# Optimization experiments

Hardware: AMD Instinct MI355X
Metric: run time of the kernel (lower is better)

The kernel has to match this reference:

```python
import jax, jax.numpy as jnp
import numpy as np
import math

B, L, D = 4, 1024, 1024
A, H = 1024, 16
DH = A // H  # head_size = 64
SCALE = 1.0 / math.sqrt(D)  # note: module scales by sqrt(input_size), not head_size
LN_EPS = 1e-5


def setup_inputs() -> dict:
    key = jax.random.key(0)
    ks = jax.random.split(key, 10)
    def xavier(k, fan_in, fan_out):
        lim = math.sqrt(6.0 / (fan_in + fan_out))
        return jax.random.uniform(k, (fan_out, fan_in), jnp.float32, -lim, lim)
    return {
        "x": jax.random.normal(ks[0], (B, L, D), jnp.float32),
        "queries": jax.random.normal(ks[1], (B, L, D), jnp.float32),
        "Wk": xavier(ks[2], D, A),
        "Wq_self": xavier(ks[3], D, A),
        "Wq_other": xavier(ks[4], D, A),
        "Wv": xavier(ks[5], D, A),
        "Wo": xavier(ks[6], A, A),
        "bo": jnp.zeros((A,), jnp.float32),
        "gamma": jnp.ones((A,), jnp.float32),
        "beta": jnp.zeros((A,), jnp.float32),
        "attention_mask": jnp.ones((B, L), jnp.int32),
    }


def reference(x, queries, Wk, Wq_self, Wq_other, Wv, Wo, bo, gamma, beta, attention_mask):
    # projections (Linear: y = x @ W.T), split heads to (B, L, H, DH)
    def proj(inp, W):
        return (inp @ W.T).reshape(B, L, H, DH)
    k = proj(x, Wk)
    q_self = proj(x, Wq_self)
    q_other = proj(queries, Wq_other)
    v = proj(x, Wv)

    # scores_self + scores_other == (q_self + q_other) @ k^T  (algebraically identical)
    q_comb = q_self + q_other
    scores = jnp.einsum("bqhd,bkhd->bhqk", q_comb, k) * SCALE  # (B, H, L, L)

    # mask: (B, L) -> (B, 1, 1, L) broadcast over heads and query positions
    m = attention_mask.astype(scores.dtype)[:, None, None, :]
    scores = scores + (1.0 - m) * -100000.0

    attn = jax.nn.softmax(scores, axis=-1)  # dropout p=0 -> identity

    out = jnp.einsum("bhqk,bkhd->bqhd", attn, v).reshape(B, L, A)

    # FF output: Linear -> identity activation -> LayerNorm (dropout=0)
    out = out @ Wo.T + bo
    mu = jnp.mean(out, axis=-1, keepdims=True)
    var = jnp.var(out, axis=-1, keepdims=True)
    out = (out - mu) * jax.lax.rsqrt(var + LN_EPS) * gamma + beta
    return out
```

## Files before the change

kernel.cpp:

```cpp
#include <hip/hip_runtime.h>
#include <hip/hip_bf16.h>
#include <math.h>

#define BB 4
#define LL 1024
#define DD 1024
#define AA 1024
#define HH 16
#define DHH 64
#define LOG2E 1.44269504f
#define QSC 0.045084223f
#define MBIAS -144269.5f

typedef __attribute__((ext_vector_type(8))) short short8;
typedef __attribute__((ext_vector_type(4))) float floatx4;

__device__ __forceinline__ float bf2f(unsigned short u) {
    union { unsigned u; float f; } x; x.u = ((unsigned)u) << 16; return x.f;
}
__device__ __forceinline__ unsigned short f2bf(float f) {
    union { float f; unsigned u; } x; x.f = f;
    unsigned r = x.u + 0x7fffu + ((x.u >> 16) & 1u);
    return (unsigned short)(r >> 16);
}
__device__ __forceinline__ unsigned pkbf(float a, float b) {
    union { __hip_bfloat162 h; unsigned u; } c;
    c.h = __float22bfloat162_rn(make_float2(a, b));
    return c.u;
}

__device__ __forceinline__ void gload16(const void* g, const void* l) {
    __builtin_amdgcn_global_load_lds(
        (const __attribute__((address_space(1))) unsigned int*)g,
        (__attribute__((address_space(3))) unsigned int*)l, 16, 0, 0);
}

__device__ __forceinline__ void remap8(int& bx, int& by) {
    const int lin = blockIdx.x + (blockIdx.y << 4);
    const int xcd = lin & 7, f = lin >> 3;
    by = ((xcd >> 1) << 3) + (f >> 3);
    bx = ((xcd & 1) << 3) + (f & 7);
}

struct ConvDesc { const float* s[8]; unsigned short* d[8]; };

__global__ __launch_bounds__(256) void conv_f2b(ConvDesc cd) {
    const int u  = blockIdx.x >> 10;
    const int lb = blockIdx.x & 1023;
    const int idx = lb * 1024 + threadIdx.x * 4;
    float4 v = *reinterpret_cast<const float4*>(cd.s[u] + idx);
    uint2 o;
    o.x = pkbf(v.x, v.y);
    o.y = pkbf(v.z, v.w);
    *reinterpret_cast<uint2*>(cd.d[u] + idx) = o;
}

__device__ __forceinline__ void gemm_pass(const unsigned short* A, const float* B,
                                          int mblk, int nblk,
                                          int kbase, int ksteps,
                                          unsigned short* As, unsigned short* Bs,
                                          floatx4 (&acc)[4][2])
{
    const int tid  = threadIdx.x;
    const int lane = tid & 63;
    const int l16  = lane & 15;
    const int quad = lane >> 4;
    const int wave = tid >> 6;
    const int wm = wave >> 1, wn = wave & 1;
    const int arow = wave * 8 + (lane >> 3);
    const int acol = ((lane & 7) ^ (lane >> 3)) << 3;
    const int brow = tid >> 3;
    const int bcol = (tid & 7) << 3;
    const int bslot = ((tid & 7) ^ (brow & 7)) << 3;

    float4 br[4];
    {
        const float* p0 = B + (size_t)(nblk + brow) * DD + kbase + bcol;
        const float* p1 = B + (size_t)(nblk + brow + 32) * DD + kbase + bcol;
        br[0] = ((const float4*)p0)[0]; br[1] = ((const float4*)p0)[1];
        br[2] = ((const float4*)p1)[0]; br[3] = ((const float4*)p1)[1];
    }

    for (int s = 0; s < ksteps; ++s) {
        const int k0 = kbase + s * 64;
        __syncthreads();
        for (int is = 0; is < 4; ++is)
            gload16(A + (size_t)(mblk + is * 32 + arow) * DD + k0 + acol,
                    As + is * 2048 + wave * 512);
        {
            uint4 t0, t1;
            t0.x = pkbf(br[0].x, br[0].y); t0.y = pkbf(br[0].z, br[0].w);
            t0.z = pkbf(br[1].x, br[1].y); t0.w = pkbf(br[1].z, br[1].w);
            t1.x = pkbf(br[2].x, br[2].y); t1.y = pkbf(br[2].z, br[2].w);
            t1.z = pkbf(br[3].x, br[3].y); t1.w = pkbf(br[3].z, br[3].w);
            *reinterpret_cast<uint4*>(Bs + brow * 64 + bslot) = t0;
            *reinterpret_cast<uint4*>(Bs + (brow + 32) * 64 + bslot) = t1;
        }
        __syncthreads();
        if (s + 1 < ksteps) {
            const int nk = k0 + 64;
            const float* p0 = B + (size_t)(nblk + brow) * DD + nk + bcol;
            const float* p1 = B + (size_t)(nblk + brow + 32) * DD + nk + bcol;
            br[0] = ((const float4*)p0)[0]; br[1] = ((const float4*)p0)[1];
            br[2] = ((const float4*)p1)[0]; br[3] = ((const float4*)p1)[1];
        }
        for (int kh = 0; kh < 2; ++kh) {
            const int sl = ((kh * 4 + quad) ^ (l16 & 7)) << 3;
            short8 af[4], bfr[2];
            for (int i = 0; i < 4; ++i)
                af[i] = *reinterpret_cast<const short8*>(
                    As + (wm * 64 + i * 16 + l16) * 64 + sl);
            for (int j = 0; j < 2; ++j)
                bfr[j] = *reinterpret_cast<const short8*>(
                    Bs + (wn * 32 + j * 16 + l16) * 64 + sl);
            for (int i = 0; i < 4; ++i)
                for (int j = 0; j < 2; ++j)
                    acc[i][j] = __builtin_amdgcn_mfma_f32_16x16x32_bf16(
                        af[i], bfr[j], acc[i][j], 0, 0, 0);
        }
    }
}

__device__ __forceinline__ void store_nat(floatx4 (&acc)[4][2], unsigned short* As,
                                          unsigned short* C, int mblk, int nblk)
{
    const int lane = threadIdx.x & 63;
    const int l16  = lane & 15;
    const int quad = lane >> 4;
    const int wave = threadIdx.x >> 6;
    const int wm = wave >> 1, wn = wave & 1;
    __syncthreads();
    unsigned short* Cw = As + wave * 2048;
    for (int i = 0; i < 4; ++i)
        for (int j = 0; j < 2; ++j)
            for (int r = 0; r < 4; ++r)
                Cw[(i * 16 + quad * 4 + r) * 32 + j * 16 + l16] = f2bf(acc[i][j][r]);
    __asm__ volatile("s_waitcnt lgkmcnt(0)" ::: "memory");
    const int mb = mblk + wm * 64;
    const int nb = nblk + wn * 32;
    for (int s = 0; s < 4; ++s) {
        const int row = s * 16 + (lane >> 2);
        uint4 v = *reinterpret_cast<const uint4*>(Cw + row * 32 + (lane & 3) * 8);
        *reinterpret_cast<uint4*>(C + (size_t)(mb + row) * AA + nb + (lane & 3) * 8) = v;
    }
}

__device__ __forceinline__ void store_vt(floatx4 (&acc)[4][2], unsigned short* As,
                                         unsigned short* vt, int mblk, int h)
{
    const int lane = threadIdx.x & 63;
    const int l16  = lane & 15;
    const int quad = lane >> 4;
    const int wave = threadIdx.x >> 6;
    const int wm = wave >> 1, wn = wave & 1;
    __syncthreads();
    unsigned short* Cw = As + wave * 2048;
    for (int i = 0; i < 4; ++i)
        for (int j = 0; j < 2; ++j) {
            ushort4 pv;
            pv.x = f2bf(acc[i][j][0]); pv.y = f2bf(acc[i][j][1]);
            pv.z = f2bf(acc[i][j][2]); pv.w = f2bf(acc[i][j][3]);
            *reinterpret_cast<ushort4*>(&Cw[(j * 16 + l16) * 64 + i * 16 + quad * 4]) = pv;
        }
    __asm__ volatile("s_waitcnt lgkmcnt(0)" ::: "memory");
    const int mg = mblk + wm * 64;
    const int b  = mg >> 10, lbase = mg & 1023;
    for (int s = 0; s < 4; ++s) {
        const int drow = s * 8 + (lane >> 3);
        uint4 v = *reinterpret_cast<const uint4*>(Cw + drow * 64 + (lane & 7) * 8);
        *reinterpret_cast<uint4*>(
            vt + (size_t)((b * HH + h) * DHH + wn * 32 + drow) * LL + lbase + (lane & 7) * 8) = v;
    }
}

__global__ __launch_bounds__(256) void gemm_proj3(
    const unsigned short* __restrict__ xb, const unsigned short* __restrict__ qb,
    const float* __restrict__ Wqs, const float* __restrict__ Wqo,
    const float* __restrict__ Wk, const float* __restrict__ Wv,
    unsigned short* __restrict__ qc, unsigned short* __restrict__ kk,
    unsigned short* __restrict__ vt)
{
    __shared__ alignas(16) unsigned short As[128 * 64];
    __shared__ alignas(16) unsigned short Bs[64 * 64];
    floatx4 acc[4][2] = {};
    int bx, by; remap8(bx, by);
    const int mblk = by * 128, nblk = bx * 64;
    if (blockIdx.z == 0) {
        gemm_pass(xb, Wqs, mblk, nblk, 0, 16, As, Bs, acc);
        gemm_pass(qb, Wqo, mblk, nblk, 0, 16, As, Bs, acc);
        store_nat(acc, As, qc, mblk, nblk);
    } else if (blockIdx.z == 1) {
        gemm_pass(xb, Wk, mblk, nblk, 0, 16, As, Bs, acc);
        store_nat(acc, As, kk, mblk, nblk);
    } else {
        gemm_pass(xb, Wv, mblk, nblk, 0, 16, As, Bs, acc);
        store_vt(acc, As, vt, mblk, bx);
    }
}

__global__ __launch_bounds__(256) void gemm_projqk(
    const unsigned short* __restrict__ xb, const unsigned short* __restrict__ qb,
    const float* __restrict__ Wqs, const float* __restrict__ Wqo,
    const float* __restrict__ Wk,
    unsigned short* __restrict__ qc, unsigned short* __restrict__ kk)
{
    __shared__ alignas(16) unsigned short As[128 * 64];
    __shared__ alignas(16) unsigned short Bs[64 * 64];
    floatx4 acc[4][2] = {};
    int bx, by; remap8(bx, by);
    const int mblk = by * 128, nblk = bx * 64;
    if (blockIdx.z == 0) {
        gemm_pass(xb, Wqs, mblk, nblk, 0, 16, As, Bs, acc);
        gemm_pass(qb, Wqo, mblk, nblk, 0, 16, As, Bs, acc);
        store_nat(acc, As, qc, mblk, nblk);
    } else {
        gemm_pass(xb, Wk, mblk, nblk, 0, 16, As, Bs, acc);
        store_nat(acc, As, kk, mblk, nblk);
    }
}

__global__ __launch_bounds__(256) void gemm_v(
    const unsigned short* __restrict__ xb, const float* __restrict__ Wv,
    unsigned short* __restrict__ vt)
{
    __shared__ alignas(16) unsigned short As[128 * 64];
    __shared__ alignas(16) unsigned short Bs[64 * 64];
    floatx4 acc[4][2] = {};
    int bx, by; remap8(bx, by);
    gemm_pass(xb, Wv, by * 128, bx * 64, 0, 16, As, Bs, acc);
    store_vt(acc, As, vt, by * 128, bx);
}

__global__ __launch_bounds__(256) void gemm_wo(
    const unsigned short* __restrict__ ao, const float* __restrict__ Wo,
    unsigned short* __restrict__ pj0, unsigned short* __restrict__ pj1)
{
    __shared__ alignas(16) unsigned short As[128 * 64];
    __shared__ alignas(16) unsigned short Bs[64 * 64];
    floatx4 acc[4][2] = {};
    int bx, by; remap8(bx, by);
    const int z = blockIdx.z;
    gemm_pass(ao, Wo, by * 128, bx * 64, z * 512, 8, As, Bs, acc);
    store_nat(acc, As, z ? pj1 : pj0, by * 128, bx * 64);
}

__device__ __forceinline__ int swzb(int row, int slot) {
    return (row << 7) + ((slot ^ (row & 7)) << 4);
}

__global__ __launch_bounds__(256, 4) void attn_flash(const unsigned short* qc,
                                                     const unsigned short* __restrict__ kmat,
                                                     const unsigned short* __restrict__ vt,
                                                     const int* __restrict__ mask,
                                                     unsigned short* ao)
{
    const int blk = blockIdx.x;
    const int xcd = blk & 7;
    const int sub = blk >> 3;
    const int bh  = xcd * 8 + (sub >> 4);
    const int qt  = sub & 15;
    const int b   = bh >> 4;
    const int h   = bh & 15;

    const int wave = threadIdx.x >> 6;
    const int lane = threadIdx.x & 63;
    const int l16  = lane & 15;
    const int quad = lane >> 4;
    const int q0 = qt * 64 + wave * 16;

    __shared__ alignas(16) unsigned short Ks[2][64 * 64];
    __shared__ alignas(16) unsigned short Vs[2][64 * 64];
    __shared__ float Ml[LL];

    const int* bm = mask + b * LL;
    for (int i = 0; i < 4; ++i) {
        const int c = threadIdx.x + i * 256;
        Ml[c] = (1.0f - (float)bm[c]) * MBIAS;
    }

    short8 aq[2];
    for (int s = 0; s < 2; ++s) {
        const unsigned short* p =
            qc + (size_t)(b * LL + q0 + l16) * AA + h * DHH + s * 32 + quad * 8;
        short8 t = *reinterpret_cast<const short8*>(p);
        for (int e = 0; e < 8; ++e)
            t[e] = (short)f2bf(bf2f((unsigned short)t[e]) * QSC);
        aq[s] = t;
    }

    floatx4 O[4] = {};
    float lp = 0.f;

    const unsigned short* kbase = kmat + (size_t)(b * LL) * AA + h * DHH;
    const unsigned short* vbase = vt + (size_t)((b * HH + h) * DHH) * LL;
    const int c0 = threadIdx.x, c1 = threadIdx.x + 256;
    const int row0 = c0 >> 3, slot0 = c0 & 7;
    const int row1 = c1 >> 3, slot1 = c1 & 7;

    uint4 kr0, kr1, vr0, vr1;
    kr0 = *reinterpret_cast<const uint4*>(kbase + (size_t)row0 * AA + slot0 * 8);
    kr1 = *reinterpret_cast<const uint4*>(kbase + (size_t)row1 * AA + slot1 * 8);
    vr0 = *reinterpret_cast<const uint4*>(vbase + (size_t)row0 * LL + slot0 * 8);
    vr1 = *reinterpret_cast<const uint4*>(vbase + (size_t)row1 * LL + slot1 * 8);
    *reinterpret_cast<uint4*>((char*)Ks[0] + swzb(row0, slot0)) = kr0;
    *reinterpret_cast<uint4*>((char*)Ks[0] + swzb(row1, slot1)) = kr1;
    *reinterpret_cast<uint4*>((char*)Vs[0] + swzb(row0, slot0)) = vr0;
    *reinterpret_cast<uint4*>((char*)Vs[0] + swzb(row1, slot1)) = vr1;
    {
        const unsigned short* kb1 = kbase + (size_t)64 * AA;
        const unsigned short* vb1 = vbase + 64;
        kr0 = *reinterpret_cast<const uint4*>(kb1 + (size_t)row0 * AA + slot0 * 8);
        kr1 = *reinterpret_cast<const uint4*>(kb1 + (size_t)row1 * AA + slot1 * 8);
        vr0 = *reinterpret_cast<const uint4*>(vb1 + (size_t)row0 * LL + slot0 * 8);
        vr1 = *reinterpret_cast<const uint4*>(vb1 + (size_t)row1 * LL + slot1 * 8);
    }
    __syncthreads();

    const int srcA = ((quad & 1) << 5) + l16;
    const int srcB = srcA + 16;
    const bool hi = quad >= 2;
    int cur = 0;

    for (int t = 0; t < 16; ++t) {
        const char* Kc = (const char*)Ks[cur];
        const char* Vc = (const char*)Vs[cur];
        if (t + 1 < 16) {
            char* Kn = (char*)Ks[cur ^ 1];
            char* Vn = (char*)Vs[cur ^ 1];
            *reinterpret_cast<uint4*>(Kn + swzb(row0, slot0)) = kr0;
            *reinterpret_cast<uint4*>(Kn + swzb(row1, slot1)) = kr1;
            *reinterpret_cast<uint4*>(Vn + swzb(row0, slot0)) = vr0;
            *reinterpret_cast<uint4*>(Vn + swzb(row1, slot1)) = vr1;
        }
        if (t + 2 < 16) {
            const unsigned short* kb2 = kbase + (size_t)(t + 2) * 64 * AA;
            const unsigned short* vb2 = vbase + (t + 2) * 64;
            kr0 = *reinterpret_cast<const uint4*>(kb2 + (size_t)row0 * AA + slot0 * 8);
            kr1 = *reinterpret_cast<const uint4*>(kb2 + (size_t)row1 * AA + slot1 * 8);
            vr0 = *reinterpret_cast<const uint4*>(vb2 + (size_t)row0 * LL + slot0 * 8);
            vr1 = *reinterpret_cast<const uint4*>(vb2 + (size_t)row1 * LL + slot1 * 8);
        }

        floatx4 p[4];
        const float* Mlb = Ml + t * 64 + quad * 4;
        for (int j = 0; j < 4; ++j) {
            const int rr = j * 16 + l16;
            const short8 kf0 = *reinterpret_cast<const short8*>(Kc + swzb(rr, quad));
            const short8 kf1 = *reinterpret_cast<const short8*>(Kc + swzb(rr, quad + 4));
            floatx4 s_ = {0.f, 0.f, 0.f, 0.f};
            s_ = __builtin_amdgcn_mfma_f32_16x16x32_bf16(kf0, aq[0], s_, 0, 0, 0);
            s_ = __builtin_amdgcn_mfma_f32_16x16x32_bf16(kf1, aq[1], s_, 0, 0, 0);
            const float4 mv = *reinterpret_cast<const float4*>(Mlb + j * 16);
            p[j][0] = exp2f(s_[0] + mv.x);
            p[j][1] = exp2f(s_[1] + mv.y);
            p[j][2] = exp2f(s_[2] + mv.z);
            p[j][3] = exp2f(s_[3] + mv.w);
            lp += (p[j][0] + p[j][1]) + (p[j][2] + p[j][3]);
        }
        unsigned pk[4][2];
        for (int j = 0; j < 4; ++j) {
            pk[j][0] = pkbf(p[j][0], p[j][1]);
            pk[j][1] = pkbf(p[j][2], p[j][3]);
        }
        union { unsigned u[4]; short8 s; } ap0, ap1;
        {
            unsigned xA0 = __shfl((int)pk[0][0], srcA), yA0 = __shfl((int)pk[1][0], srcA);
            unsigned xA1 = __shfl((int)pk[0][1], srcA), yA1 = __shfl((int)pk[1][1], srcA);
            unsigned xB0 = __shfl((int)pk[0][0], srcB), yB0 = __shfl((int)pk[1][0], srcB);
            unsigned xB1 = __shfl((int)pk[0][1], srcB), yB1 = __shfl((int)pk[1][1], srcB);
            ap0.u[0] = hi ? yA0 : xA0;
            ap0.u[1] = hi ? yA1 : xA1;
            ap0.u[2] = hi ? yB0 : xB0;
            ap0.u[3] = hi ? yB1 : xB1;
        }
        {
            unsigned xA0 = __shfl((int)pk[2][0], srcA), yA0 = __shfl((int)pk[3][0], srcA);
            unsigned xA1 = __shfl((int)pk[2][1], srcA), yA1 = __shfl((int)pk[3][1], srcA);
            unsigned xB0 = __shfl((int)pk[2][0], srcB), yB0 = __shfl((int)pk[3][0], srcB);
            unsigned xB1 = __shfl((int)pk[2][1], srcB), yB1 = __shfl((int)pk[3][1], srcB);
            ap1.u[0] = hi ? yA0 : xA0;
            ap1.u[1] = hi ? yA1 : xA1;
            ap1.u[2] = hi ? yB0 : xB0;
            ap1.u[3] = hi ? yB1 : xB1;
        }
        for (int t4 = 0; t4 < 4; ++t4) {
            const int rr = t4 * 16 + l16;
            const short8 bv0 = *reinterpret_cast<const short8*>(Vc + swzb(rr, quad));
            const short8 bv1 = *reinterpret_cast<const short8*>(Vc + swzb(rr, quad + 4));
            O[t4] = __builtin_amdgcn_mfma_f32_16x16x32_bf16(ap0.s, bv0, O[t4], 0, 0, 0);
            O[t4] = __builtin_amdgcn_mfma_f32_16x16x32_bf16(ap1.s, bv1, O[t4], 0, 0, 0);
        }
        __syncthreads();
        cur ^= 1;
    }

    lp += __shfl_xor(lp, 16);
    lp += __shfl_xor(lp, 32);
    float linv[4];
    for (int r = 0; r < 4; ++r) {
        const float s = __shfl(lp, quad * 4 + r);
        linv[r] = 1.0f / s;
    }
    for (int t4 = 0; t4 < 4; ++t4)
        for (int r = 0; r < 4; ++r)
            ao[(size_t)(b * LL + q0 + quad * 4 + r) * AA + h * DHH + t4 * 16 + l16] =
                f2bf(O[t4][r] * linv[r]);
}

__global__ __launch_bounds__(256) void ln_f32(const unsigned short* __restrict__ X0,
                                              const unsigned short* __restrict__ X1,
                                              const float* __restrict__ bo,
                                              const float* __restrict__ gamma,
                                              const float* __restrict__ beta,
                                              float* __restrict__ out)
{
    const int row = blockIdx.x;
    const unsigned short* x0 = X0 + (size_t)row * AA;
    const unsigned short* x1 = X1 + (size_t)row * AA;
    float v[4];
    float s = 0.f, s2 = 0.f;
    for (int e = 0; e < 4; ++e) {
        const int c = threadIdx.x + e * 256;
        const float f = bf2f(x0[c]) + bf2f(x1[c]) + bo[c];
        v[e] = f; s += f; s2 += f * f;
    }
    for (int d = 1; d < 64; d <<= 1) { s += __shfl_xor(s, d); s2 += __shfl_xor(s2, d); }
    __shared__ float red[4][2];
    const int wave = threadIdx.x >> 6;
    const int lane = threadIdx.x & 63;
    if (lane == 0) { red[wave][0] = s; red[wave][1] = s2; }
    __syncthreads();
    s  = red[0][0] + red[1][0] + red[2][0] + red[3][0];
    s2 = red[0][1] + red[1][1] + red[2][1] + red[3][1];
    const float mean = s * (1.0f / AA);
    const float var  = s2 * (1.0f / AA) - mean * mean;
    const float rstd = rsqrtf(var + 1e-5f);
    for (int e = 0; e < 4; ++e) {
        const int c = threadIdx.x + e * 256;
        out[(size_t)row * AA + c] = (v[e] - mean) * rstd * gamma[c] + beta[c];
    }
}

extern "C" void kernel_launch(void* const* d_in, const int* in_sizes, int n_in,
                              void* d_out, int out_size, void* d_ws, size_t ws_size,
                              hipStream_t stream)
{
    const float* x     = (const float*)d_in[0];
    const float* qrs   = (const float*)d_in[1];
    const float* Wk    = (const float*)d_in[2];
    const float* Wqs   = (const float*)d_in[3];
    const float* Wqo   = (const float*)d_in[4];
    const float* Wv    = (const float*)d_in[5];
    const float* Wo    = (const float*)d_in[6];
    const float* bo    = (const float*)d_in[7];
    const float* gamma = (const float*)d_in[8];
    const float* beta  = (const float*)d_in[9];
    const int*   mask  = (const int*)d_in[10];

    char* ws = (char*)d_ws;
    unsigned short* xb = (unsigned short*)(ws + (size_t)0);
    unsigned short* qb = (unsigned short*)(ws + ((size_t)8 << 20));
    const bool big = ws_size >= ((size_t)24 << 20);
    unsigned short* vt = big ? (unsigned short*)(ws + ((size_t)16 << 20)) : qb;
    unsigned short* qc = (unsigned short*)d_out;
    unsigned short* kk = (unsigned short*)((char*)d_out + ((size_t)8 << 20));
    unsigned short* ao  = qc;
    unsigned short* pj0 = xb;
    unsigned short* pj1 = kk;

    ConvDesc cd;
    for (int i = 0; i < 4; ++i) {
        cd.s[i]     = x   + (size_t)i * (1u << 20); cd.d[i]     = xb + (size_t)i * (1u << 20);
        cd.s[i + 4] = qrs + (size_t)i * (1u << 20); cd.d[i + 4] = qb + (size_t)i * (1u << 20);
    }
    conv_f2b<<<8 * 1024, 256, 0, stream>>>(cd);

    if (big) {
        dim3 g3(AA / 64, (BB * LL) / 128, 3);
        gemm_proj3<<<g3, 256, 0, stream>>>(xb, qb, Wqs, Wqo, Wk, Wv, qc, kk, vt);
    } else {
        dim3 g2(AA / 64, (BB * LL) / 128, 2);
        dim3 g1(AA / 64, (BB * LL) / 128);
        gemm_projqk<<<g2, 256, 0, stream>>>(xb, qb, Wqs, Wqo, Wk, qc, kk);
        gemm_v<<<g1, 256, 0, stream>>>(xb, Wv, vt);
    }
    attn_flash<<<BB * HH * (LL / 64), 256, 0, stream>>>(qc, kk, vt, mask, ao);
    dim3 gw(AA / 64, (BB * LL) / 128, 2);
    gemm_wo<<<gw, 256, 0, stream>>>(ao, Wo, pj0, pj1);
    ln_f32<<<BB * LL, 256, 0, stream>>>(pj0, pj1, bo, gamma, beta, (float*)d_out);
}
```

Before: 235.4 us.

## Widen projection GEMM tiles to 128x128 with per-wave 64x64 outputs

```diff
diff --git a/kernel.cpp b/kernel.cpp
--- a/kernel.cpp
+++ b/kernel.cpp
@@ -42,6 +42,13 @@
     bx = ((xcd & 1) << 3) + (f & 7);
 }
 
+__device__ __forceinline__ void remap128(int& bx, int& by) {
+    const int lin = blockIdx.x + (blockIdx.y << 3);
+    const int xcd = lin & 7, f = lin >> 3;
+    bx = ((xcd & 1) << 2) + (f & 3);
+    by = ((xcd >> 1) << 3) + (f >> 2);
+}
+
 struct ConvDesc { const float* s[8]; unsigned short* d[8]; };
 
 __global__ __launch_bounds__(256) void conv_f2b(ConvDesc cd) {
@@ -53,6 +60,195 @@
     o.x = pkbf(v.x, v.y);
     o.y = pkbf(v.z, v.w);
     *reinterpret_cast<uint2*>(cd.d[u] + idx) = o;
+}
+
+__device__ __forceinline__ void gemm_pass128(const unsigned short* A, const float* B,
+                                             int mblk, int nblk,
+                                             int kbase, int ksteps,
+                                             unsigned short* As, unsigned short* Bs,
+                                             floatx4 (&acc)[4][4])
+{
+    const int tid  = threadIdx.x;
+    const int lane = tid & 63;
+    const int l16  = lane & 15;
+    const int quad = lane >> 4;
+    const int wave = tid >> 6;
+    const int wm = wave >> 1, wn = wave & 1;
+    const int arow = wave * 8 + (lane >> 3);
+    const int acol = ((lane & 7) ^ (lane >> 3)) << 3;
+    const int brow = tid >> 3;
+    const int bcol = (tid & 7) << 3;
+    const int bslot = ((tid & 7) ^ (brow & 7)) << 3;
+
+    const unsigned short* ap = A + (size_t)(mblk + arow) * DD + kbase + acol;
+    const float* bp0 = B + (size_t)(nblk + brow) * DD + kbase + bcol;
+    const float* bp1 = bp0 + (size_t)32 * DD;
+    const float* bp2 = bp0 + (size_t)64 * DD;
+    const float* bp3 = bp0 + (size_t)96 * DD;
+
+    float4 br[8];
+    br[0] = ((const float4*)bp0)[0]; br[1] = ((const float4*)bp0)[1];
+    br[2] = ((const float4*)bp1)[0]; br[3] = ((const float4*)bp1)[1];
+    br[4] = ((const float4*)bp2)[0]; br[5] = ((const float4*)bp2)[1];
+    br[6] = ((const float4*)bp3)[0]; br[7] = ((const float4*)bp3)[1];
+
+    for (int s = 0; s < ksteps; ++s) {
+        __syncthreads();
+        for (int is = 0; is < 4; ++is)
+            gload16(ap + (size_t)(is * 32) * DD, As + is * 2048 + wave * 512);
+        {
+            uint4 t;
+            t.x = pkbf(br[0].x, br[0].y); t.y = pkbf(br[0].z, br[0].w);
+            t.z = pkbf(br[1].x, br[1].y); t.w = pkbf(br[1].z, br[1].w);
+            *reinterpret_cast<uint4*>(Bs + brow * 64 + bslot) = t;
+            t.x = pkbf(br[2].x, br[2].y); t.y = pkbf(br[2].z, br[2].w);
+            t.z = pkbf(br[3].x, br[3].y); t.w = pkbf(br[3].z, br[3].w);
+            *reinterpret_cast<uint4*>(Bs + (brow + 32) * 64 + bslot) = t;
+            t.x = pkbf(br[4].x, br[4].y); t.y = pkbf(br[4].z, br[4].w);
+            t.z = pkbf(br[5].x, br[5].y); t.w = pkbf(br[5].z, br[5].w);
+            *reinterpret_cast<uint4*>(Bs + (brow + 64) * 64 + bslot) = t;
+            t.x = pkbf(br[6].x, br[6].y); t.y = pkbf(br[6].z, br[6].w);
+            t.z = pkbf(br[7].x, br[7].y); t.w = pkbf(br[7].z, br[7].w);
+            *reinterpret_cast<uint4*>(Bs + (brow + 96) * 64 + bslot) = t;
+        }
+        __syncthreads();
+        if (s + 1 < ksteps) {
+            bp0 += 64; bp1 += 64; bp2 += 64; bp3 += 64;
+            br[0] = ((const float4*)bp0)[0]; br[1] = ((const float4*)bp0)[1];
+            br[2] = ((const float4*)bp1)[0]; br[3] = ((const float4*)bp1)[1];
+            br[4] = ((const float4*)bp2)[0]; br[5] = ((const float4*)bp2)[1];
+            br[6] = ((const float4*)bp3)[0]; br[7] = ((const float4*)bp3)[1];
+        }
+        ap += 64;
+        for (int kh = 0; kh < 2; ++kh) {
+            const int sl = ((kh * 4 + quad) ^ (l16 & 7)) << 3;
+            short8 af[4], bfr[4];
+            for (int i = 0; i < 4; ++i)
+                af[i] = *reinterpret_cast<const short8*>(
+                    As + (wm * 64 + i * 16 + l16) * 64 + sl);
+            for (int j = 0; j < 4; ++j)
+                bfr[j] = *reinterpret_cast<const short8*>(
+                    Bs + (wn * 64 + j * 16 + l16) * 64 + sl);
+            for (int i = 0; i < 4; ++i)
+                for (int j = 0; j < 4; ++j)
+                    acc[i][j] = __builtin_amdgcn_mfma_f32_16x16x32_bf16(
+                        af[i], bfr[j], acc[i][j], 0, 0, 0);
+        }
+    }
+}
+
+__device__ __forceinline__ void store_nat128(floatx4 (&acc)[4][4], unsigned short* S,
+                                             unsigned short* C, int mblk, int nblk)
+{
+    const int lane = threadIdx.x & 63;
+    const int l16  = lane & 15;
+    const int quad = lane >> 4;
+    const int wave = threadIdx.x >> 6;
+    const int wm = wave >> 1, wn = wave & 1;
+    __syncthreads();
+    unsigned short* Cw = S + wave * 4096;
+    for (int i = 0; i < 4; ++i)
+        for (int j = 0; j < 4; ++j)
+            for (int r = 0; r < 4; ++r)
+                Cw[(i * 16 + quad * 4 + r) * 64 + j * 16 + l16] = f2bf(acc[i][j][r]);
+    __asm__ volatile("s_waitcnt lgkmcnt(0)" ::: "memory");
+    const int mb = mblk + wm * 64;
+    const int nb = nblk + wn * 64;
+    for (int s = 0; s < 8; ++s) {
+        const int row = s * 8 + (lane >> 3);
+        uint4 v = *reinterpret_cast<const uint4*>(Cw + row * 64 + (lane & 7) * 8);
+        *reinterpret_cast<uint4*>(C + (size_t)(mb + row) * AA + nb + (lane & 7) * 8) = v;
+    }
+}
+
+__device__ __forceinline__ void store_vt128(floatx4 (&acc)[4][4], unsigned short* S,
+                                            unsigned short* vt, int mblk, int nblk)
+{
+    const int lane = threadIdx.x & 63;
+    const int l16  = lane & 15;
+    const int quad = lane >> 4;
+    const int wave = threadIdx.x >> 6;
+    const int wm = wave >> 1, wn = wave & 1;
+    __syncthreads();
+    unsigned short* Cw = S + wave * 4096;
+    for (int i = 0; i < 4; ++i)
+        for (int j = 0; j < 4; ++j) {
+            ushort4 pv;
+            pv.x = f2bf(acc[i][j][0]); pv.y = f2bf(acc[i][j][1]);
+            pv.z = f2bf(acc[i][j][2]); pv.w = f2bf(acc[i][j][3]);
+            *reinterpret_cast<ushort4*>(&Cw[(j * 16 + l16) * 64 + i * 16 + quad * 4]) = pv;
+        }
+    __asm__ volatile("s_waitcnt lgkmcnt(0)" ::: "memory");
+    const int mg = mblk + wm * 64;
+    const int b  = mg >> 10, lbase = mg & 1023;
+    const int h  = (nblk >> 6) + wn;
+    for (int s = 0; s < 8; ++s) {
+        const int drow = s * 8 + (lane >> 3);
+        uint4 v = *reinterpret_cast<const uint4*>(Cw + drow * 64 + (lane & 7) * 8);
+        *reinterpret_cast<uint4*>(
+            vt + (size_t)((b * HH + h) * DHH + drow) * LL + lbase + (lane & 7) * 8) = v;
+    }
+}
+
+__global__ __launch_bounds__(256, 3) void gemm_proj3(
+    const unsigned short* __restrict__ xb, const unsigned short* __restrict__ qb,
+    const float* __restrict__ Wqs, const float* __restrict__ Wqo,
+    const float* __restrict__ Wk, const float* __restrict__ Wv,
+    unsigned short* __restrict__ qc, unsigned short* __restrict__ kk,
+    unsigned short* __restrict__ vt)
+{
+    __shared__ alignas(16) unsigned short S[128 * 64 * 2];
+    unsigned short* As = S;
+    unsigned short* Bs = S + 128 * 64;
+    floatx4 acc[4][4] = {};
+    int bx, by; remap128(bx, by);
+    const int mblk = by * 128, nblk = bx * 128;
+    if (blockIdx.z == 0) {
+        gemm_pass128(xb, Wqs, mblk, nblk, 0, 16, As, Bs, acc);
+        gemm_pass128(qb, Wqo, mblk, nblk, 0, 16, As, Bs, acc);
+        store_nat128(acc, S, qc, mblk, nblk);
+    } else if (blockIdx.z == 1) {
+        gemm_pass128(xb, Wk, mblk, nblk, 0, 16, As, Bs, acc);
+        store_nat128(acc, S, kk, mblk, nblk);
+    } else {
+        gemm_pass128(xb, Wv, mblk, nblk, 0, 16, As, Bs, acc);
+        store_vt128(acc, S, vt, mblk, nblk);
+    }
+}
+
+__global__ __launch_bounds__(256, 3) void gemm_projqk(
+    const unsigned short* __restrict__ xb, const unsigned short* __restrict__ qb,
+    const float* __restrict__ Wqs, const float* __restrict__ Wqo,
+    const float* __restrict__ Wk,
+    unsigned short* __restrict__ qc, unsigned short* __restrict__ kk)
+{
+    __shared__ alignas(16) unsigned short S[128 * 64 * 2];
+    unsigned short* As = S;
+    unsigned short* Bs = S + 128 * 64;
+    floatx4 acc[4][4] = {};
+    int bx, by; remap128(bx, by);
+    const int mblk = by * 128, nblk = bx * 128;
+    if (blockIdx.z == 0) {
+        gemm_pass128(xb, Wqs, mblk, nblk, 0, 16, As, Bs, acc);
+        gemm_pass128(qb, Wqo, mblk, nblk, 0, 16, As, Bs, acc);
+        store_nat128(acc, S, qc, mblk, nblk);
+    } else {
+        gemm_pass128(xb, Wk, mblk, nblk, 0, 16, As, Bs, acc);
+        store_nat128(acc, S, kk, mblk, nblk);
+    }
+}
+
+__global__ __launch_bounds__(256, 3) void gemm_v(
+    const unsigned short* __restrict__ xb, const float* __restrict__ Wv,
+    unsigned short* __restrict__ vt)
+{
+    __shared__ alignas(16) unsigned short S[128 * 64 * 2];
+    unsigned short* As = S;
+    unsigned short* Bs = S + 128 * 64;
+    floatx4 acc[4][4] = {};
+    int bx, by; remap128(bx, by);
+    gemm_pass128(xb, Wv, by * 128, bx * 128, 0, 16, As, Bs, acc);
+    store_vt128(acc, S, vt, by * 128, bx * 128);
 }
 
 __device__ __forceinline__ void gemm_pass(const unsigned short* A, const float* B,
@@ -145,92 +341,6 @@
     }
 }
 
-__device__ __forceinline__ void store_vt(floatx4 (&acc)[4][2], unsigned short* As,
-                                         unsigned short* vt, int mblk, int h)
-{
-    const int lane = threadIdx.x & 63;
-    const int l16  = lane & 15;
-    const int quad = lane >> 4;
-    const int wave = threadIdx.x >> 6;
-    const int wm = wave >> 1, wn = wave & 1;
-    __syncthreads();
-    unsigned short* Cw = As + wave * 2048;
-    for (int i = 0; i < 4; ++i)
-        for (int j = 0; j < 2; ++j) {
-            ushort4 pv;
-            pv.x = f2bf(acc[i][j][0]); pv.y = f2bf(acc[i][j][1]);
-            pv.z = f2bf(acc[i][j][2]); pv.w = f2bf(acc[i][j][3]);
-            *reinterpret_cast<ushort4*>(&Cw[(j * 16 + l16) * 64 + i * 16 + quad * 4]) = pv;
-        }
-    __asm__ volatile("s_waitcnt lgkmcnt(0)" ::: "memory");
-    const int mg = mblk + wm * 64;
-    const int b  = mg >> 10, lbase = mg & 1023;
-    for (int s = 0; s < 4; ++s) {
-        const int drow = s * 8 + (lane >> 3);
-        uint4 v = *reinterpret_cast<const uint4*>(Cw + drow * 64 + (lane & 7) * 8);
-        *reinterpret_cast<uint4*>(
-            vt + (size_t)((b * HH + h) * DHH + wn * 32 + drow) * LL + lbase + (lane & 7) * 8) = v;
-    }
-}
-
-__global__ __launch_bounds__(256) void gemm_proj3(
-    const unsigned short* __restrict__ xb, const unsigned short* __restrict__ qb,
-    const float* __restrict__ Wqs, const float* __restrict__ Wqo,
-    const float* __restrict__ Wk, const float* __restrict__ Wv,
-    unsigned short* __restrict__ qc, unsigned short* __restrict__ kk,
-    unsigned short* __restrict__ vt)
-{
-    __shared__ alignas(16) unsigned short As[128 * 64];
-    __shared__ alignas(16) unsigned short Bs[64 * 64];
-    floatx4 acc[4][2] = {};
-    int bx, by; remap8(bx, by);
-    const int mblk = by * 128, nblk = bx * 64;
-    if (blockIdx.z == 0) {
-        gemm_pass(xb, Wqs, mblk, nblk, 0, 16, As, Bs, acc);
-        gemm_pass(qb, Wqo, mblk, nblk, 0, 16, As, Bs, acc);
-        store_nat(acc, As, qc, mblk, nblk);
-    } else if (blockIdx.z == 1) {
-        gemm_pass(xb, Wk, mblk, nblk, 0, 16, As, Bs, acc);
-        store_nat(acc, As, kk, mblk, nblk);
-    } else {
-        gemm_pass(xb, Wv, mblk, nblk, 0, 16, As, Bs, acc);
-        store_vt(acc, As, vt, mblk, bx);
-    }
-}
-
-__global__ __launch_bounds__(256) void gemm_projqk(
-    const unsigned short* __restrict__ xb, const unsigned short* __restrict__ qb,
-    const float* __restrict__ Wqs, const float* __restrict__ Wqo,
-    const float* __restrict__ Wk,
-    unsigned short* __restrict__ qc, unsigned short* __restrict__ kk)
-{
-    __shared__ alignas(16) unsigned short As[128 * 64];
-    __shared__ alignas(16) unsigned short Bs[64 * 64];
-    floatx4 acc[4][2] = {};
-    int bx, by; remap8(bx, by);
-    const int mblk = by * 128, nblk = bx * 64;
-    if (blockIdx.z == 0) {
-        gemm_pass(xb, Wqs, mblk, nblk, 0, 16, As, Bs, acc);
-        gemm_pass(qb, Wqo, mblk, nblk, 0, 16, As, Bs, acc);
-        store_nat(acc, As, qc, mblk, nblk);
-    } else {
-        gemm_pass(xb, Wk, mblk, nblk, 0, 16, As, Bs, acc);
-        store_nat(acc, As, kk, mblk, nblk);
-    }
-}
-
-__global__ __launch_bounds__(256) void gemm_v(
-    const unsigned short* __restrict__ xb, const float* __restrict__ Wv,
-    unsigned short* __restrict__ vt)
-{
-    __shared__ alignas(16) unsigned short As[128 * 64];
-    __shared__ alignas(16) unsigned short Bs[64 * 64];
-    floatx4 acc[4][2] = {};
-    int bx, by; remap8(bx, by);
-    gemm_pass(xb, Wv, by * 128, bx * 64, 0, 16, As, Bs, acc);
-    store_vt(acc, As, vt, by * 128, bx);
-}
-
 __global__ __launch_bounds__(256) void gemm_wo(
     const unsigned short* __restrict__ ao, const float* __restrict__ Wo,
     unsigned short* __restrict__ pj0, unsigned short* __restrict__ pj1)
@@ -476,11 +586,11 @@
     conv_f2b<<<8 * 1024, 256, 0, stream>>>(cd);
 
     if (big) {
-        dim3 g3(AA / 64, (BB * LL) / 128, 3);
+        dim3 g3(AA / 128, (BB * LL) / 128, 3);
         gemm_proj3<<<g3, 256, 0, stream>>>(xb, qb, Wqs, Wqo, Wk, Wv, qc, kk, vt);
     } else {
-        dim3 g2(AA / 64, (BB * LL) / 128, 2);
-        dim3 g1(AA / 64, (BB * LL) / 128);
+        dim3 g2(AA / 128, (BB * LL) / 128, 2);
+        dim3 g1(AA / 128, (BB * LL) / 128);
         gemm_projqk<<<g2, 256, 0, stream>>>(xb, qb, Wqs, Wqo, Wk, qc, kk);
         gemm_v<<<g1, 256, 0, stream>>>(xb, Wv, vt);
     }
```

After: 240.6 us. 1.02x slower.
